# Kernel tuning notes

Measured on AMD Instinct MI355X. Metric: run time of the kernel, lower is better.

## Reference

```python
import jax, jax.numpy as jnp
import numpy as np

K_POS, K_NEG = 3, 2
MIN_D = 9  # min_dist=8 bumped to next odd, as in _nms_topk
BN_EPS = 1e-5


def _conv(x, w, pad):
    return jax.lax.conv_general_dilated(
        x, w, (1, 1), [(pad, pad), (pad, pad)],
        dimension_numbers=('NCHW', 'OIHW', 'NCHW'))


def _bn(x, g, b, m, v):
    scale = g * jax.lax.rsqrt(v + BN_EPS)  # inference-mode BN
    return x * scale[None, :, None, None] + (b - m * scale)[None, :, None, None]


def _head(x, w1, g1, b1, m1, v1, w2, g2, b2, m2, v2, w3, b3, out_hw):
    h = jax.nn.relu(_bn(_conv(x, w1, 1), g1, b1, m1, v1))
    h = jax.nn.relu(_bn(_conv(h, w2, 1), g2, b2, m2, v2))
    logits = _conv(h, w3, 0) + b3[None, :, None, None]
    B = logits.shape[0]
    # F.interpolate(mode='bilinear', align_corners=False) == half-pixel bilinear resize
    logits = jax.image.resize(logits, (B, 1, out_hw, out_hw), method='bilinear')
    return logits


def _sample_one(smap, key):
    # smap: [H, W] sigmoid heatmap for one sample
    H, W = smap.shape
    # --- positive points: NMS-style peak top-k ---
    local_max = jax.lax.reduce_window(
        smap, -jnp.inf, jax.lax.max, (MIN_D, MIN_D), (1, 1), 'SAME')
    is_peak = (smap == local_max) & (smap > 0.1)
    masked = jnp.where(is_peak, smap, -jnp.inf).reshape(-1)
    vals, idx = jax.lax.top_k(masked, K_POS)
    valid = jnp.isfinite(vals)  # slots corresponding to real peaks
    xs = jnp.where(valid, (idx % W).astype(jnp.float32), 0.0)
    ys = jnp.where(valid, (idx // W).astype(jnp.float32), 0.0)
    pos_lab = jnp.where(valid, 1, -1).astype(jnp.int32)
    # fallback: no peak at all -> single argmax point in slot 0
    amax = jnp.argmax(smap)
    any_peak = valid[0]
    xs = xs.at[0].set(jnp.where(any_peak, xs[0], (amax % W).astype(jnp.float32)))
    ys = ys.at[0].set(jnp.where(any_peak, ys[0], (amax // W).astype(jnp.float32)))
    pos_lab = pos_lab.at[0].set(1)  # slot 0 is always a positive point
    pos = jnp.stack([xs, ys], axis=1)  # [K_POS, 2] (x, y)
    # --- negative points: uniform sample from low-response region ---
    low = (smap < 0.3).reshape(-1)
    low_fb = (smap < smap.max()).reshape(-1)
    mask = jnp.where(jnp.any(low), low, low_fb)
    n = mask.sum()
    # stable argsort puts masked-in (True) flat indices first, in index order
    order = jnp.argsort(jnp.logical_not(mask))
    u = jax.random.uniform(key, (K_NEG,))
    ridx = jnp.minimum((u * jnp.maximum(n, 1).astype(jnp.float32)).astype(jnp.int32),
                       jnp.maximum(n - 1, 0))
    sel = order[ridx]
    neg = jnp.stack([sel % W, sel // W], axis=1).astype(jnp.float32)
    neg = jnp.where(n > 0, neg, jnp.zeros_like(neg))
    neg_lab = jnp.zeros((K_NEG,), jnp.int32)
    coords = jnp.concatenate([pos, neg], axis=0)      # [K_POS+K_NEG, 2]
    labels = jnp.concatenate([pos_lab, neg_lab], axis=0)
    return coords, labels


def setup_inputs() -> dict:
    key = jax.random.key(0)
    ks = jax.random.split(key, 4)
    B, C, h, w = 32, 256, 64, 64
    HID = 64
    x = jax.random.normal(ks[0], (B, C, h, w), jnp.float32)
    w1 = jax.random.normal(ks[1], (HID, C, 3, 3), jnp.float32) * 0.03  # kaiming-ish
    w2 = jax.random.normal(ks[2], (HID, HID, 3, 3), jnp.float32) * 0.06
    w3 = jax.random.normal(ks[3], (1, HID, 1, 1), jnp.float32) * 0.17
    b3 = jnp.full((1,), -2.0, jnp.float32)
    ones = jnp.ones((HID,), jnp.float32)
    zeros = jnp.zeros((HID,), jnp.float32)
    return {
        'encoder_features': x,
        'w1': w1, 'g1': ones, 'b1': zeros, 'm1': zeros, 'v1': ones,
        'w2': w2, 'g2': ones, 'b2': zeros, 'm2': zeros, 'v2': ones,
        'w3': w3, 'b3': b3,
        'output_size': 256,
    }


def reference(encoder_features, w1, g1, b1, m1, v1, w2, g2, b2, m2, v2, w3, b3, output_size):
    logits = _head(encoder_features, w1, g1, b1, m1, v1, w2, g2, b2, m2, v2, w3, b3, output_size)
    heatmap = jax.nn.sigmoid(logits)  # [B, 1, H, W]
    B = heatmap.shape[0]
    keys = jax.random.split(jax.random.key(42), B)
    coords, labels = jax.vmap(_sample_one)(heatmap[:, 0], keys)
    point_coords = coords[:, None].astype(jnp.float32)  # [B, 1, K, 2]
    point_labels = labels[:, None].astype(jnp.int32)    # [B, 1, K]
    return heatmap, point_coords, point_labels, logits
```

## Files before the change

kernel.cpp:

```cpp
#include <hip/hip_runtime.h>
#include <stdint.h>
#include <math.h>

#define NEG_INF (-__builtin_inff())
#define IDX_SENT 0x7fffffff

__device__ __forceinline__ void threefry2x32(uint32_t k0, uint32_t k1,
                                             uint32_t x0, uint32_t x1,
                                             uint32_t* o0, uint32_t* o1) {
  const uint32_t ks2 = k0 ^ k1 ^ 0x1BD11BDAu;
  uint32_t ks[3] = {k0, k1, ks2};
  const int rot[2][4] = {{13, 15, 26, 6}, {17, 29, 16, 24}};
  x0 += ks[0];
  x1 += ks[1];
#pragma unroll
  for (int i = 0; i < 5; ++i) {
#pragma unroll
    for (int j = 0; j < 4; ++j) {
      const int r = rot[i & 1][j];
      x0 += x1;
      x1 = (x1 << r) | (x1 >> (32 - r));
      x1 ^= x0;
    }
    x0 += ks[(i + 1) % 3];
    x1 += ks[(i + 2) % 3] + (uint32_t)(i + 1);
  }
  *o0 = x0;
  *o1 = x1;
}

__device__ __forceinline__ float bits_to_uniform(uint32_t bits) {
  return __uint_as_float((bits >> 9) | 0x3f800000u) - 1.0f;
}

__device__ __forceinline__ void top3_insert(float v, int idx, float tv[3], int ti[3]) {
  if ((v > tv[2]) || (v == tv[2] && idx < ti[2])) {
    tv[2] = v; ti[2] = idx;
    if ((tv[2] > tv[1]) || (tv[2] == tv[1] && ti[2] < ti[1])) {
      float fv = tv[1]; int fi = ti[1];
      tv[1] = tv[2]; ti[1] = ti[2];
      tv[2] = fv;     ti[2] = fi;
      if ((tv[1] > tv[0]) || (tv[1] == tv[0] && ti[1] < ti[0])) {
        fv = tv[0]; fi = ti[0];
        tv[0] = tv[1]; ti[0] = ti[1];
        tv[1] = fv;    ti[1] = fi;
      }
    }
  }
}

__global__ __launch_bounds__(256) void transpose_w4(
    const float* __restrict__ w, float* __restrict__ wt, int IC9) {
  const int idx = blockIdx.x * 256 + threadIdx.x;
  const int qrow = idx >> 6;
  const int oc = idx & 63;
  const float4 v = *(const float4*)&w[(size_t)oc * IC9 + qrow * 4];
  wt[(size_t)(qrow * 4 + 0) * 64 + oc] = v.x;
  wt[(size_t)(qrow * 4 + 1) * 64 + oc] = v.y;
  wt[(size_t)(qrow * 4 + 2) * 64 + oc] = v.z;
  wt[(size_t)(qrow * 4 + 3) * 64 + oc] = v.w;
}

template <int IC>
__global__ __launch_bounds__(256, 4) void conv3x3_bn_relu(
    const float* __restrict__ x, const float* __restrict__ wt,
    const float* __restrict__ g, const float* __restrict__ bb,
    const float* __restrict__ m, const float* __restrict__ vv,
    float* __restrict__ out) {
  __shared__ float xs[8][10][20];

  const int tid = threadIdx.x;
  const int blk = blockIdx.x;
  const int b = blk >> 5;
  const int tile = blk & 31;
  const int by = (tile >> 2) << 3;
  const int bx = (tile & 3) << 4;
  const int wv = __builtin_amdgcn_readfirstlane(tid >> 6);
  const int lane = tid & 63;
  const int r = lane >> 3;
  const int lc = (lane & 7) << 1;
  const int ocbase = wv << 4;

  const int sic = tid >> 5;
  const int sc = tid & 31;
  const int gx = bx + sc - 1;
  const bool cok = (sc < 18) && (gx >= 0) && (gx < 64);

  float acc[2][16];
#pragma unroll
  for (int p = 0; p < 2; ++p)
#pragma unroll
    for (int o = 0; o < 16; ++o) acc[p][o] = 0.0f;

  for (int icb = 0; icb < IC; icb += 8) {
    const float* xp = x + ((size_t)b * IC + icb + sic) * 4096;
#pragma unroll
    for (int rr = 0; rr < 10; ++rr) {
      const int gy = by + rr - 1;
      float val = 0.0f;
      if (cok && gy >= 0 && gy < 64) val = xp[gy * 64 + gx];
      if (sc < 18) xs[sic][rr][sc] = val;
    }
    __syncthreads();

    const float* wbase = wt + (size_t)icb * 9 * 64 + ocbase;
    for (int ic = 0; ic < 8; ++ic) {
#pragma unroll
      for (int ky = 0; ky < 3; ++ky) {
        float xv[4];
        *(float2*)&xv[0] = *(const float2*)&xs[ic][r + ky][lc];
        *(float2*)&xv[2] = *(const float2*)&xs[ic][r + ky][lc + 2];
#pragma unroll
        for (int kx = 0; kx < 3; ++kx) {
          const float4* wp4 = (const float4*)(wbase + (ic * 9 + ky * 3 + kx) * 64);
#pragma unroll
          for (int q = 0; q < 4; ++q) {
            const float4 w4 = wp4[q];
            acc[0][4 * q + 0] = fmaf(xv[kx],     w4.x, acc[0][4 * q + 0]);
            acc[1][4 * q + 0] = fmaf(xv[kx + 1], w4.x, acc[1][4 * q + 0]);
            acc[0][4 * q + 1] = fmaf(xv[kx],     w4.y, acc[0][4 * q + 1]);
            acc[1][4 * q + 1] = fmaf(xv[kx + 1], w4.y, acc[1][4 * q + 1]);
            acc[0][4 * q + 2] = fmaf(xv[kx],     w4.z, acc[0][4 * q + 2]);
            acc[1][4 * q + 2] = fmaf(xv[kx + 1], w4.z, acc[1][4 * q + 2]);
            acc[0][4 * q + 3] = fmaf(xv[kx],     w4.w, acc[0][4 * q + 3]);
            acc[1][4 * q + 3] = fmaf(xv[kx + 1], w4.w, acc[1][4 * q + 3]);
          }
        }
      }
    }
    __syncthreads();
  }

#pragma unroll
  for (int o = 0; o < 16; ++o) {
    const int oc = ocbase + o;
    const float sc2 = g[oc] * (1.0f / sqrtf(vv[oc] + 1e-5f));
    const float sh = bb[oc] - m[oc] * sc2;
    float2 v;
    v.x = fmaxf(fmaf(acc[0][o], sc2, sh), 0.0f);
    v.y = fmaxf(fmaf(acc[1][o], sc2, sh), 0.0f);
    *(float2*)&out[(((size_t)b * 64 + oc) * 64 + (by + r)) * 64 + bx + lc] = v;
  }
}

__global__ __launch_bounds__(256) void logits64_k(
    const float* __restrict__ h2, const float* __restrict__ w3,
    const float* __restrict__ b3, float* __restrict__ lg64) {
  const int blk = blockIdx.x;
  const int b = blk >> 4;
  const int p = ((blk & 15) << 8) + threadIdx.x;
  __shared__ float wvv[64];
  if (threadIdx.x < 64) wvv[threadIdx.x] = w3[threadIdx.x];
  __syncthreads();
  float s = b3[0];
  const float* hp = h2 + (size_t)b * 64 * 4096 + p;
  for (int oc = 0; oc < 64; ++oc)
    s = fmaf(hp[(size_t)oc * 4096], wvv[oc], s);
  lg64[b * 4096 + p] = s;
}

__global__ __launch_bounds__(256) void upsample_k(
    const float* __restrict__ lg64, float* __restrict__ logits,
    float* __restrict__ heat) {
  const int blk = blockIdx.x;
  const int b = blk >> 6;
  const int qq = ((blk & 63) << 10) + (threadIdx.x << 2);
  const float* lg = lg64 + b * 4096;
  const int oy = qq >> 8;
  const float sy = (float)oy * 0.25f - 0.375f;
  const float fy = floorf(sy);
  const int y0 = (int)fy;
  const float ty = sy - fy;
  const int y0c = y0 < 0 ? 0 : y0;
  const int y1c = (y0 + 1) > 63 ? 63 : (y0 + 1);
  const float* r0 = lg + y0c * 64;
  const float* r1 = lg + y1c * 64;
  float4 lo, he;
  float* lop = (float*)&lo;
  float* hep = (float*)&he;
#pragma unroll
  for (int j = 0; j < 4; ++j) {
    const int ox = (qq & 255) + j;
    const float sx = (float)ox * 0.25f - 0.375f;
    const float fx = floorf(sx);
    const int x0 = (int)fx;
    const float tx = sx - fx;
    const int x0c = x0 < 0 ? 0 : x0;
    const int x1c = (x0 + 1) > 63 ? 63 : (x0 + 1);
    const float v00 = r0[x0c], v01 = r0[x1c];
    const float v10 = r1[x0c], v11 = r1[x1c];
    const float vtop = v00 + (v01 - v00) * tx;
    const float vbot = v10 + (v11 - v10) * tx;
    const float val = vtop + (vbot - vtop) * ty;
    lop[j] = val;
    hep[j] = 1.0f / (1.0f + expf(-val));
  }
  const size_t o = (size_t)b * 65536 + qq;
  *(float4*)(logits + o) = lo;
  *(float4*)(heat + o) = he;
}

__global__ __launch_bounds__(256) void pos_stripe(
    const float* __restrict__ heat, float* __restrict__ cand) {
  const int b = blockIdx.x >> 4;
  const int stripe = blockIdx.x & 15;
  const int y0 = stripe << 4;
  const float* s = heat + (size_t)b * 65536;
  const int tid = threadIdx.x;
  __shared__ float sm[24][256];
  __shared__ float rm[24][256];
  __shared__ float rv[256 * 3];
  __shared__ int ri[256 * 3];
  __shared__ float mvv[256];
  __shared__ int mii[256];
  __shared__ float rv2[24];
  __shared__ int ri2[24];
  __shared__ float mv2[8];
  __shared__ int mi2[8];

  for (int l = tid; l < 24 * 256; l += 256) {
    const int rr = l >> 8, xx = l & 255;
    const int gy = y0 - 4 + rr;
    sm[rr][xx] = (gy >= 0 && gy < 256) ? s[gy * 256 + xx] : NEG_INF;
  }
  __syncthreads();
  for (int l = tid; l < 24 * 256; l += 256) {
    const int rr = l >> 8, xx = l & 255;
    const int lo = (xx - 4 < 0) ? 0 : xx - 4;
    const int hi = (xx + 4 > 255) ? 255 : xx + 4;
    float mx = NEG_INF;
    for (int x2 = lo; x2 <= hi; ++x2) mx = fmaxf(mx, sm[rr][x2]);
    rm[rr][xx] = mx;
  }
  __syncthreads();

  float tv[3] = {NEG_INF, NEG_INF, NEG_INF};
  int ti[3] = {IDX_SENT, IDX_SENT, IDX_SENT};
  float bmax = NEG_INF;
  int bidx = IDX_SENT;
  for (int l = tid; l < 16 * 256; l += 256) {
    const int ry = l >> 8, xx = l & 255;
    const int lr = ry + 4;
    const float v = sm[lr][xx];
    float lm = rm[lr - 4][xx];
#pragma unroll
    for (int d = -3; d <= 4; ++d) lm = fmaxf(lm, rm[lr + d][xx]);
    const int gidx = (y0 + ry) * 256 + xx;
    if (v > bmax) { bmax = v; bidx = gidx; }
    if (v == lm && v > 0.1f) top3_insert(v, gidx, tv, ti);
  }

  rv[tid * 3 + 0] = tv[0]; rv[tid * 3 + 1] = tv[1]; rv[tid * 3 + 2] = tv[2];
  ri[tid * 3 + 0] = ti[0]; ri[tid * 3 + 1] = ti[1]; ri[tid * 3 + 2] = ti[2];
  mvv[tid] = bmax; mii[tid] = bidx;
  __syncthreads();

  if (tid < 8) {
    float av[3] = {NEG_INF, NEG_INF, NEG_INF};
    int ai[3] = {IDX_SENT, IDX_SENT, IDX_SENT};
    float am = NEG_INF; int amI = IDX_SENT;
    for (int t = tid * 32; t < tid * 32 + 32; ++t) {
      for (int k = 0; k < 3; ++k) top3_insert(rv[t * 3 + k], ri[t * 3 + k], av, ai);
      if (mvv[t] > am || (mvv[t] == am && mii[t] < amI)) { am = mvv[t]; amI = mii[t]; }
    }
    rv2[tid * 3 + 0] = av[0]; rv2[tid * 3 + 1] = av[1]; rv2[tid * 3 + 2] = av[2];
    ri2[tid * 3 + 0] = ai[0]; ri2[tid * 3 + 1] = ai[1]; ri2[tid * 3 + 2] = ai[2];
    mv2[tid] = am; mi2[tid] = amI;
  }
  __syncthreads();

  if (tid == 0) {
    float fv[3] = {NEG_INF, NEG_INF, NEG_INF};
    int fi[3] = {IDX_SENT, IDX_SENT, IDX_SENT};
    for (int t = 0; t < 24; ++t) top3_insert(rv2[t], ri2[t], fv, fi);
    float gbv = NEG_INF; int gbi = IDX_SENT;
    for (int t = 0; t < 8; ++t)
      if (mv2[t] > gbv || (mv2[t] == gbv && mi2[t] < gbi)) { gbv = mv2[t]; gbi = mi2[t]; }
    float* c = cand + ((size_t)b * 16 + stripe) * 8;
    c[0] = fv[0]; c[1] = __int_as_float(fi[0]);
    c[2] = fv[1]; c[3] = __int_as_float(fi[1]);
    c[4] = fv[2]; c[5] = __int_as_float(fi[2]);
    c[6] = gbv;   c[7] = __int_as_float(gbi);
  }
}

__global__ void pos_final(const float* __restrict__ cand,
                          float* __restrict__ coords, float* __restrict__ labels) {
  const int b = blockIdx.x;
  if (threadIdx.x != 0) return;
  float fv[3] = {NEG_INF, NEG_INF, NEG_INF};
  int fi[3] = {IDX_SENT, IDX_SENT, IDX_SENT};
  float gbv = NEG_INF; int gbi = IDX_SENT;
  for (int st = 0; st < 16; ++st) {
    const float* c = cand + ((size_t)b * 16 + st) * 8;
    for (int k = 0; k < 3; ++k)
      top3_insert(c[2 * k], __float_as_int(c[2 * k + 1]), fv, fi);
    const float mv = c[6]; const int mi = __float_as_int(c[7]);
    if (mv > gbv || (mv == gbv && mi < gbi)) { gbv = mv; gbi = mi; }
  }
  float* co = coords + (size_t)b * 10;
  float* la = labels + (size_t)b * 5;
  const bool any_peak = (fi[0] != IDX_SENT);
  const int i0 = any_peak ? fi[0] : gbi;
  co[0] = (float)(i0 & 255);
  co[1] = (float)(i0 >> 8);
  la[0] = 1.0f;
  for (int k = 1; k < 3; ++k) {
    const bool valid = (fi[k] != IDX_SENT);
    co[k * 2 + 0] = valid ? (float)(fi[k] & 255) : 0.0f;
    co[k * 2 + 1] = valid ? (float)(fi[k] >> 8) : 0.0f;
    la[k] = valid ? 1.0f : -1.0f;
  }
}

__global__ __launch_bounds__(256) void neg_count(
    const float* __restrict__ heat, float* __restrict__ ncnt,
    float* __restrict__ pmax) {
  const int blk = blockIdx.x;
  const int b = blk >> 2;
  const int part = blk & 3;
  const int tid = threadIdx.x;
  const int chunk = (part << 8) + tid;
  const float4* s = (const float4*)(heat + (size_t)b * 65536 + chunk * 64);
  int c = 0;
  float mx = NEG_INF;
  for (int i = 0; i < 16; ++i) {
    const float4 v = s[i];
    c += (v.x < 0.3f) + (v.y < 0.3f) + (v.z < 0.3f) + (v.w < 0.3f);
    mx = fmaxf(mx, fmaxf(fmaxf(v.x, v.y), fmaxf(v.z, v.w)));
  }
  ncnt[b * 1024 + chunk] = (float)c;
  __shared__ float mxs[256];
  mxs[tid] = mx;
  __syncthreads();
  if (tid == 0) {
    float gmx = NEG_INF;
    for (int t = 0; t < 256; ++t) gmx = fmaxf(gmx, mxs[t]);
    pmax[blk] = gmx;
  }
}

__global__ __launch_bounds__(256) void neg_select(
    const float* __restrict__ heat, const float* __restrict__ ncnt,
    const float* __restrict__ pmax, float* __restrict__ coords,
    float* __restrict__ labels) {
  const int b = blockIdx.x;
  const int tid = threadIdx.x;
  const float* s = heat + (size_t)b * 65536;
  __shared__ float cnt[1024];
  __shared__ float c256[256];
  __shared__ int pfx[257];
  __shared__ float thr_s;
  __shared__ int fb_s;
  __shared__ int n_s;
  __shared__ int ridx_s[2];

  for (int l = tid; l < 1024; l += 256) cnt[l] = ncnt[b * 1024 + l];
  __syncthreads();
  c256[tid] = cnt[4 * tid] + cnt[4 * tid + 1] + cnt[4 * tid + 2] + cnt[4 * tid + 3];
  __syncthreads();
  if (tid == 0) {
    int tot = 0;
    for (int t = 0; t < 256; ++t) tot += (int)c256[t];
    const float gm = fmaxf(fmaxf(pmax[b * 4], pmax[b * 4 + 1]),
                           fmaxf(pmax[b * 4 + 2], pmax[b * 4 + 3]));
    fb_s = (tot > 0) ? 0 : 1;
    thr_s = (tot > 0) ? 0.3f : gm;
  }
  __syncthreads();
  if (fb_s) {
    const float t2 = thr_s;
    const int base = tid * 256;
    int c = 0;
    for (int i = 0; i < 256; ++i) c += (s[base + i] < t2) ? 1 : 0;
    c256[tid] = (float)c;
    __syncthreads();
  }
  if (tid == 0) {
    int run = 0;
    for (int t = 0; t < 256; ++t) { pfx[t] = run; run += (int)c256[t]; }
    pfx[256] = run;
    const int n = run;
    n_s = n;
    uint32_t k0, k1, a0, a1;
    threefry2x32(0u, 42u, 0u, (uint32_t)b, &k0, &k1);
    threefry2x32(k0, k1, 0u, 0u, &a0, &a1);
    const uint32_t bits0 = a0 ^ a1;
    threefry2x32(k0, k1, 0u, 1u, &a0, &a1);
    const uint32_t bits1 = a0 ^ a1;
    const float u0 = bits_to_uniform(bits0);
    const float u1 = bits_to_uniform(bits1);
    const float nf = (float)(n > 1 ? n : 1);
    int r0 = (int)(u0 * nf);
    int r1 = (int)(u1 * nf);
    const int rmax = (n - 1 > 0) ? n - 1 : 0;
    ridx_s[0] = r0 < rmax ? r0 : rmax;
    ridx_s[1] = r1 < rmax ? r1 : rmax;
    labels[(size_t)b * 5 + 3] = 0.0f;
    labels[(size_t)b * 5 + 4] = 0.0f;
    if (n == 0) {
      coords[(size_t)b * 10 + 6] = 0.0f; coords[(size_t)b * 10 + 7] = 0.0f;
      coords[(size_t)b * 10 + 8] = 0.0f; coords[(size_t)b * 10 + 9] = 0.0f;
    }
  }
  __syncthreads();
  const int n = n_s;
  if (n > 0) {
    const float t2 = thr_s;
    const int p0 = pfx[tid], p1 = pfx[tid + 1];
    const int base = tid * 256;
    for (int j = 0; j < 2; ++j) {
      const int r = ridx_s[j];
      if (r >= p0 && r < p1) {
        int need = r - p0;
        int sel = -1;
        for (int i = 0; i < 256; ++i) {
          if (s[base + i] < t2) {
            if (need == 0) { sel = base + i; break; }
            --need;
          }
        }
        coords[(size_t)b * 10 + 6 + j * 2 + 0] = (float)(sel & 255);
        coords[(size_t)b * 10 + 6 + j * 2 + 1] = (float)(sel >> 8);
      }
    }
  }
}

extern "C" void kernel_launch(void* const* d_in, const int* in_sizes, int n_in,
                              void* d_out, int out_size, void* d_ws, size_t ws_size,
                              hipStream_t stream) {
  (void)in_sizes; (void)n_in; (void)out_size; (void)ws_size;
  const float* x  = (const float*)d_in[0];
  const float* w1 = (const float*)d_in[1];
  const float* g1 = (const float*)d_in[2];
  const float* b1 = (const float*)d_in[3];
  const float* m1 = (const float*)d_in[4];
  const float* v1 = (const float*)d_in[5];
  const float* w2 = (const float*)d_in[6];
  const float* g2 = (const float*)d_in[7];
  const float* b2 = (const float*)d_in[8];
  const float* m2 = (const float*)d_in[9];
  const float* v2 = (const float*)d_in[10];
  const float* w3 = (const float*)d_in[11];
  const float* b3 = (const float*)d_in[12];

  float* out = (float*)d_out;
  float* heat = out;
  float* coords = out + (size_t)32 * 65536;
  float* labels = coords + 320;
  float* logits = labels + 160;

  float* w1t = logits;
  float* w2t = logits + 147456;

  float* h1 = (float*)d_ws;
  float* h2 = h1 + (size_t)32 * 64 * 64 * 64;
  float* lg64 = h1;
  float* cand = h1 + 131072;
  float* ncnt = h1 + 135168;
  float* pmax = h1 + 167936;

  transpose_w4<<<144, 256, 0, stream>>>(w1, w1t, 2304);
  transpose_w4<<<36, 256, 0, stream>>>(w2, w2t, 576);
  conv3x3_bn_relu<256><<<1024, 256, 0, stream>>>(x, w1t, g1, b1, m1, v1, h1);
  conv3x3_bn_relu<64><<<1024, 256, 0, stream>>>(h1, w2t, g2, b2, m2, v2, h2);
  logits64_k<<<512, 256, 0, stream>>>(h2, w3, b3, lg64);
  upsample_k<<<2048, 256, 0, stream>>>(lg64, logits, heat);
  pos_stripe<<<512, 256, 0, stream>>>(heat, cand);
  pos_final<<<32, 64, 0, stream>>>(cand, coords, labels);
  neg_count<<<128, 256, 0, stream>>>(heat, ncnt, pmax);
  neg_select<<<32, 256, 0, stream>>>(heat, ncnt, pmax, coords, labels);
}
```

Measured before the change: 826.3 us.

## Double-buffer conv input tiles with register prefetch and remap lanes for LDS

```diff
diff --git a/kernel.cpp b/kernel.cpp
--- a/kernel.cpp
+++ b/kernel.cpp
@@ -67,7 +67,7 @@
     const float* __restrict__ g, const float* __restrict__ bb,
     const float* __restrict__ m, const float* __restrict__ vv,
     float* __restrict__ out) {
-  __shared__ float xs[8][10][20];
+  __shared__ float xs[2][8][10][20];
 
   const int tid = threadIdx.x;
   const int blk = blockIdx.x;
@@ -77,8 +77,8 @@
   const int bx = (tile & 3) << 4;
   const int wv = __builtin_amdgcn_readfirstlane(tid >> 6);
   const int lane = tid & 63;
-  const int r = lane >> 3;
-  const int lc = (lane & 7) << 1;
+  const int r = lane & 7;
+  const int lc = (lane >> 3) << 1;
   const int ocbase = wv << 4;
 
   const int sic = tid >> 5;
@@ -92,24 +92,41 @@
 #pragma unroll
     for (int o = 0; o < 16; ++o) acc[p][o] = 0.0f;
 
-  for (int icb = 0; icb < IC; icb += 8) {
-    const float* xp = x + ((size_t)b * IC + icb + sic) * 4096;
+  float pre[10];
+  {
+    const float* xp = x + ((size_t)b * IC + sic) * 4096;
 #pragma unroll
     for (int rr = 0; rr < 10; ++rr) {
       const int gy = by + rr - 1;
-      float val = 0.0f;
-      if (cok && gy >= 0 && gy < 64) val = xp[gy * 64 + gx];
-      if (sc < 18) xs[sic][rr][sc] = val;
-    }
-    __syncthreads();
+      pre[rr] = 0.0f;
+      if (cok && gy >= 0 && gy < 64) pre[rr] = xp[gy * 64 + gx];
+    }
+#pragma unroll
+    for (int rr = 0; rr < 10; ++rr)
+      if (sc < 18) xs[0][sic][rr][sc] = pre[rr];
+  }
+  __syncthreads();
+
+  int cur = 0;
+  for (int icb = 0; icb < IC; icb += 8) {
+    const bool has_next = (icb + 8) < IC;
+    if (has_next) {
+      const float* xp = x + ((size_t)b * IC + icb + 8 + sic) * 4096;
+#pragma unroll
+      for (int rr = 0; rr < 10; ++rr) {
+        const int gy = by + rr - 1;
+        pre[rr] = 0.0f;
+        if (cok && gy >= 0 && gy < 64) pre[rr] = xp[gy * 64 + gx];
+      }
+    }
 
     const float* wbase = wt + (size_t)icb * 9 * 64 + ocbase;
     for (int ic = 0; ic < 8; ++ic) {
 #pragma unroll
       for (int ky = 0; ky < 3; ++ky) {
         float xv[4];
-        *(float2*)&xv[0] = *(const float2*)&xs[ic][r + ky][lc];
-        *(float2*)&xv[2] = *(const float2*)&xs[ic][r + ky][lc + 2];
+        *(float2*)&xv[0] = *(const float2*)&xs[cur][ic][r + ky][lc];
+        *(float2*)&xv[2] = *(const float2*)&xs[cur][ic][r + ky][lc + 2];
 #pragma unroll
         for (int kx = 0; kx < 3; ++kx) {
           const float4* wp4 = (const float4*)(wbase + (ic * 9 + ky * 3 + kx) * 64);
@@ -128,7 +145,14 @@
         }
       }
     }
+
+    if (has_next) {
+#pragma unroll
+      for (int rr = 0; rr < 10; ++rr)
+        if (sc < 18) xs[cur ^ 1][sic][rr][sc] = pre[rr];
+    }
     __syncthreads();
+    cur ^= 1;
   }
 
 #pragma unroll
```

Result: faster. 802.4 us (-2.9%).
